# Kernel tuning notes

Hardware: AMD Instinct MI355X
Metric: run time of the kernel (lower is better)

## Reference

```python
import jax, jax.numpy as jnp
import numpy as np

N, C, EMB_ROWS = 524288, 128, 32
SLOPE = 0.2  # leaky_relu negative slope


def setup_inputs() -> dict:
    key = jax.random.key(0)
    k1, k2, k3, k4, k5 = jax.random.split(key, 5)
    x = jax.random.normal(k1, (N, C), jnp.float32)
    perm = jax.random.permutation(k2, N)  # fixed stand-in for torch.randperm
    depth = jax.random.normal(k3, (EMB_ROWS, 128), jnp.float32)  # Embedding(32,128), N(0,1) init
    fan_in = 2 * C * 2
    bound = 1.0 / np.sqrt(fan_in)
    W = jax.random.uniform(k4, (C, 2 * C, 2), jnp.float32, -bound, bound)  # Conv1d weight (O,I,K)
    b = jax.random.uniform(k5, (C,), jnp.float32, -bound, bound)
    return {"x": x, "depth": depth, "W": W, "b": b, "perm": perm}


def reference(x, depth, W, b, perm):
    c = W.shape[0]
    x = x[perm]                      # random shuffle of rows
    x = x.T.reshape(1, c, -1)        # [1, C, N]
    i = 0
    # Python while over STATIC shapes -> unrolled at trace time (~log2(N) steps)
    while x.shape[-1] > 1:
        L = x.shape[-1]
        e = jnp.broadcast_to(depth[i].reshape(1, 128, 1), (1, 128, L))
        x = jnp.concatenate([x, e], axis=1)   # [1, 2C, L]
        x = jax.lax.conv_general_dilated(
            x, W, window_strides=(1,), padding="VALID",
            dimension_numbers=("NCH", "OIH", "NCH"))  # [1, C, L-1]
        x = x + b.reshape(1, -1, 1)
        x = jnp.where(x >= 0, x, SLOPE * x)   # leaky_relu(0.2)
        if x.shape[-1] == 1:
            break
        # MaxPool1d(2,2): floor(L/2), drops trailing element for odd L
        x = jax.lax.reduce_window(
            x, -jnp.inf, jax.lax.max,
            window_dimensions=(1, 1, 2), window_strides=(1, 1, 2),
            padding="VALID")
        i += 1
    return x.reshape(c, 1).T  # [1, C]
```

## Files before the change

kernel.cpp:

```cpp
#include <hip/hip_runtime.h>
#include <hip/hip_bf16.h>


typedef __bf16 v8bf __attribute__((ext_vector_type(8)));
typedef float v16f __attribute__((ext_vector_type(16)));

__device__ __forceinline__ ushort f2bf(float f) {
    __hip_bfloat16 h = __float2bfloat16(f);
    return *reinterpret_cast<ushort*>(&h);
}
__device__ __forceinline__ unsigned pack2(float lo, float hi) {
    return (unsigned)f2bf(lo) | ((unsigned)f2bf(hi) << 16);
}
__device__ __forceinline__ float leaky(float y) { return (y >= 0.f) ? y : 0.2f * y; }

#define ZACC {0.f,0.f,0.f,0.f,0.f,0.f,0.f,0.f,0.f,0.f,0.f,0.f,0.f,0.f,0.f,0.f}

__global__ void bias_kernel(const float* __restrict__ W, const float* __restrict__ b,
                            const float* __restrict__ depth, float* __restrict__ Bst) {
    int i = blockIdx.x, o = threadIdx.x;
    const float* Wo = W + (size_t)o * 512 + 256;
    const float* di = depth + (size_t)i * 128;
    float s = b[o];
#pragma unroll 8
    for (int c = 0; c < 128; ++c) s += di[c] * (Wo[2 * c] + Wo[2 * c + 1]);
    Bst[i * 128 + o] = s;
}

__global__ void repack_kernel(const float* __restrict__ W, ushort* __restrict__ A) {
    int o = blockIdx.x, c = threadIdx.x;
    float v = (c < 128) ? W[(size_t)o * 512 + 2 * c] : W[(size_t)o * 512 + 2 * (c - 128) + 1];
    A[o * 256 + c] = f2bf(v);
}

#define WAVE_SETUP()                                                          \
    const int tid = threadIdx.x;                                              \
    const int lane = tid & 63;                                                \
    const int w = tid >> 6;                                                   \
    const int n31 = lane & 31;                                                \
    const int h = lane >> 5;                                                  \
    v8bf af[16];                                                              \
    {                                                                         \
        const ushort* Arow = A + (size_t)(w * 32 + n31) * 256 + h * 8;        \
        _Pragma("unroll")                                                     \
        for (int s = 0; s < 16; ++s) af[s] = *(const v8bf*)&Arow[s * 16];     \
    }

#define LOAD_BIAS(dst_, Bs)                                                   \
    float dst_[16];                                                           \
    _Pragma("unroll")                                                         \
    for (int r = 0; r < 16; ++r)                                              \
        dst_[r] = (Bs)[w * 32 + (r & 3) + 8 * (r >> 2) + 4 * h];

#define MFMA_TILE_LDS(buf, r0_, r1_, acc)                                     \
    {                                                                         \
        const ushort* sp0 = (buf) + (r0_) * 128;                              \
        const ushort* sp1 = (buf) + (r1_) * 128;                              \
        const int mm0 = (r0_) & 15, mm1 = (r1_) & 15;                         \
        v16f accB_ = ZACC;                                                    \
        __builtin_amdgcn_s_setprio(1);                                        \
        _Pragma("unroll")                                                     \
        for (int s = 0; s < 8; ++s) {                                         \
            acc = __builtin_amdgcn_mfma_f32_32x32x16_bf16(                    \
                af[s], *(const v8bf*)&sp0[((2 * s + h) ^ mm0) * 8], acc, 0, 0, 0); \
            accB_ = __builtin_amdgcn_mfma_f32_32x32x16_bf16(                  \
                af[8 + s], *(const v8bf*)&sp1[((2 * s + h) ^ mm1) * 8], accB_, 0, 0, 0); \
        }                                                                     \
        __builtin_amdgcn_s_setprio(0);                                        \
        acc += accB_;                                                         \
    }

__global__ __launch_bounds__(256)
void pair_fused(const ushort* __restrict__ Xin,
                const float* __restrict__ x0,
                const int* __restrict__ perm,
                const ushort* __restrict__ A,
                const float* __restrict__ Bst2,
                ushort* __restrict__ Y,
                int Lin, int Lp2, int stage0) {
    __shared__ __align__(16) ushort xin[132 * 128];
    __shared__ __align__(16) ushort mid[65 * 128];

    const int U = blockIdx.x * 32;
    const int t0 = U * 4;

    if (stage0) {
        int pr[9];
        float4 aa[9], bb[9];
#pragma unroll
        for (int k = 0; k < 9; ++k) {
            int idx = threadIdx.x + 256 * k;
            if (idx < 132 * 16) {
                int row = idx >> 4;
                pr[k] = perm[min(t0 + row, Lin - 1)];
            }
        }
#pragma unroll
        for (int k = 0; k < 9; ++k) {
            int idx = threadIdx.x + 256 * k;
            if (idx < 132 * 16) {
                int ck = idx & 15;
                const float* s = x0 + (size_t)pr[k] * 128 + ck * 8;
                aa[k] = *(const float4*)s;
                bb[k] = *(const float4*)(s + 4);
            }
        }
#pragma unroll
        for (int k = 0; k < 9; ++k) {
            int idx = threadIdx.x + 256 * k;
            if (idx < 132 * 16) {
                int row = idx >> 4, ck = idx & 15;
                uint4 v;
                v.x = pack2(aa[k].x, aa[k].y);  v.y = pack2(aa[k].z, aa[k].w);
                v.z = pack2(bb[k].x, bb[k].y);  v.w = pack2(bb[k].z, bb[k].w);
                *(uint4*)&xin[row * 128 + ((ck ^ (row & 15)) * 8)] = v;
            }
        }
    } else {
        uint4 vv[9];
#pragma unroll
        for (int k = 0; k < 9; ++k) {
            int idx = threadIdx.x + 256 * k;
            if (idx < 132 * 16) {
                int row = idx >> 4, ck = idx & 15;
                int t = min(t0 + row, Lin - 1);
                vv[k] = *(const uint4*)&Xin[(size_t)t * 128 + ck * 8];
            }
        }
#pragma unroll
        for (int k = 0; k < 9; ++k) {
            int idx = threadIdx.x + 256 * k;
            if (idx < 132 * 16) {
                int row = idx >> 4, ck = idx & 15;
                *(uint4*)&xin[row * 128 + ((ck ^ (row & 15)) * 8)] = vv[k];
            }
        }
    }
    __syncthreads();

    WAVE_SETUP();

    {
        LOAD_BIAS(bias_r, Bst2);
#pragma unroll
        for (int ti = 0; ti < 5; ++ti) {
            const int p = 32 * ti + n31;
            const int r0 = min(p, 131), r1 = min(p + 1, 131);
            v16f acc = ZACC;
            MFMA_TILE_LDS(xin, r0, r1, acc);
            const int u1 = 16 * ti + (n31 >> 1);
            const bool act = !(lane & 1) && (u1 < 65);
#pragma unroll
            for (int q = 0; q < 4; ++q) {
                float pv[4];
#pragma unroll
                for (int j = 0; j < 4; ++j) {
                    float y = leaky(acc[4 * q + j] + bias_r[4 * q + j]);
                    float y2 = __shfl_xor(y, 1, 64);
                    pv[j] = fmaxf(y, y2);
                }
                if (act) {
                    uint2 v;
                    v.x = pack2(pv[0], pv[1]);
                    v.y = pack2(pv[2], pv[3]);
                    *(uint2*)&mid[u1 * 128 + (((4 * w + q) ^ (u1 & 15)) * 8) + 4 * h] = v;
                }
            }
        }
    }
    __syncthreads();

    {
        LOAD_BIAS(bias_r, Bst2 + 128);
#pragma unroll
        for (int ti = 0; ti < 2; ++ti) {
            const int p = 32 * ti + n31;
            v16f acc = ZACC;
            MFMA_TILE_LDS(mid, p, p + 1, acc);
            const int u2 = U + 16 * ti + (n31 >> 1);
            const bool act = !(lane & 1) && (u2 < Lp2);
#pragma unroll
            for (int q = 0; q < 4; ++q) {
                float pv[4];
#pragma unroll
                for (int j = 0; j < 4; ++j) {
                    float y = leaky(acc[4 * q + j] + bias_r[4 * q + j]);
                    float y2 = __shfl_xor(y, 1, 64);
                    pv[j] = fmaxf(y, y2);
                }
                if (act) {
                    uint2 v;
                    v.x = pack2(pv[0], pv[1]);
                    v.y = pack2(pv[2], pv[3]);
                    *(uint2*)&Y[(size_t)u2 * 128 + w * 32 + 8 * q + 4 * h] = v;
                }
            }
        }
    }
}

__global__ __launch_bounds__(256)
void tail_fused(const ushort* __restrict__ Xg, const ushort* __restrict__ A,
                const float* __restrict__ BstAll, float* __restrict__ out) {
    extern __shared__ __align__(16) ushort tbuf[];
    ushort* buf0 = tbuf;
    ushort* buf1 = tbuf + 255 * 128;

    WAVE_SETUP();

    int Lin = 511;
    for (int st = 0; st < 8; ++st) {
        const int Lp = (Lin - 1) >> 1;
        LOAD_BIAS(bias_r, BstAll + (size_t)(10 + st) * 128);
        ushort* dst = (st & 1) ? buf1 : buf0;
        const ushort* src = (st & 1) ? buf0 : buf1;
        const int ntiles = (Lin - 1 + 31) >> 5;
        for (int ti = 0; ti < ntiles; ++ti) {
            const int t = ti * 32 + n31;
            const int r0 = min(t, Lin - 1), r1 = min(t + 1, Lin - 1);
            v16f acc = ZACC;
            if (st == 0) {
                const ushort* p0 = Xg + (size_t)r0 * 128 + h * 8;
                const ushort* p1 = Xg + (size_t)r1 * 128 + h * 8;
                v16f accB = ZACC;
                __builtin_amdgcn_s_setprio(1);
#pragma unroll
                for (int s = 0; s < 8; ++s) {
                    acc = __builtin_amdgcn_mfma_f32_32x32x16_bf16(
                        af[s], *(const v8bf*)&p0[s * 16], acc, 0, 0, 0);
                    accB = __builtin_amdgcn_mfma_f32_32x32x16_bf16(
                        af[8 + s], *(const v8bf*)&p1[s * 16], accB, 0, 0, 0);
                }
                __builtin_amdgcn_s_setprio(0);
                acc += accB;
            } else {
                MFMA_TILE_LDS(src, r0, r1, acc);
            }
            const int u = t >> 1;
            const bool act = !(lane & 1) && (u < Lp);
#pragma unroll
            for (int q = 0; q < 4; ++q) {
                float pv[4];
#pragma unroll
                for (int j = 0; j < 4; ++j) {
                    float y = leaky(acc[4 * q + j] + bias_r[4 * q + j]);
                    float y2 = __shfl_xor(y, 1, 64);
                    pv[j] = fmaxf(y, y2);
                }
                if (act) {
                    if (st < 7) {
                        uint2 v;
                        v.x = pack2(pv[0], pv[1]);
                        v.y = pack2(pv[2], pv[3]);
                        *(uint2*)&dst[u * 128 + (((4 * w + q) ^ (u & 15)) * 8) + 4 * h] = v;
                    } else {
                        float4 o = {pv[0], pv[1], pv[2], pv[3]};
                        *(float4*)&out[w * 32 + 8 * q + 4 * h] = o;
                    }
                }
            }
        }
        __syncthreads();
        Lin = Lp;
    }
}

extern "C" void kernel_launch(void* const* d_in, const int* in_sizes, int n_in,
                              void* d_out, int out_size, void* d_ws, size_t ws_size,
                              hipStream_t stream) {
    const float* x     = (const float*)d_in[0];
    const float* depth = (const float*)d_in[1];
    const float* W     = (const float*)d_in[2];
    const float* b     = (const float*)d_in[3];
    const int*   perm  = (const int*)d_in[4];
    float* out = (float*)d_out;

    char* ws = (char*)d_ws;
    float*  Bst = (float*)ws;
    ushort* A   = (ushort*)(ws + 16384);
    ushort* R0  = (ushort*)(ws + 16384 + 65536);
    ushort* R1  = (ushort*)(ws + 16384 + 65536 + (size_t)131071 * 256);

    bias_kernel<<<18, 128, 0, stream>>>(W, b, depth, Bst);
    repack_kernel<<<128, 256, 0, stream>>>(W, A);

    pair_fused<<<4096, 256, 0, stream>>>(nullptr, x, perm, A, Bst, R0,
                                         524288, 131071, 1);
    pair_fused<<<1024, 256, 0, stream>>>(R0, nullptr, nullptr, A, Bst + 2 * 128, R1,
                                         131071, 32767, 0);
    pair_fused<<<256, 256, 0, stream>>>(R1, nullptr, nullptr, A, Bst + 4 * 128, R0,
                                        32767, 8191, 0);
    pair_fused<<<64, 256, 0, stream>>>(R0, nullptr, nullptr, A, Bst + 6 * 128, R1,
                                       8191, 2047, 0);
    pair_fused<<<16, 256, 0, stream>>>(R1, nullptr, nullptr, A, Bst + 8 * 128, R0,
                                       2047, 511, 0);
    tail_fused<<<1, 256, (255 + 127) * 128 * 2, stream>>>(R0, A, Bst, out);
}
```

Before: 572.5 us.

## Pre-convert input to bf16, merge prep kernels, widen tail kernel

Adds a streaming pass that converts the whole fp32 input to bf16 before the first fused stage, so the permuted gather reads half as many bytes per row. It also stages perm indices in shared memory, merges the bias and weight repack kernels into one launch, drops s_setprio hints, and doubles the tail kernel's waves so tiles are split between two wave groups. The trade-off is an extra full read of x plus a 128MB write and re-read of the bf16 copy, which may cost more than it saves in the gather.

```diff
diff --git a/kernel.cpp b/kernel.cpp
--- a/kernel.cpp
+++ b/kernel.cpp
@@ -4,6 +4,7 @@
 
 typedef __bf16 v8bf __attribute__((ext_vector_type(8)));
 typedef float v16f __attribute__((ext_vector_type(16)));
+typedef float v4f __attribute__((ext_vector_type(4)));
 
 __device__ __forceinline__ ushort f2bf(float f) {
     __hip_bfloat16 h = __float2bfloat16(f);
@@ -16,41 +17,58 @@
 
 #define ZACC {0.f,0.f,0.f,0.f,0.f,0.f,0.f,0.f,0.f,0.f,0.f,0.f,0.f,0.f,0.f,0.f}
 
-__global__ void bias_kernel(const float* __restrict__ W, const float* __restrict__ b,
-                            const float* __restrict__ depth, float* __restrict__ Bst) {
-    int i = blockIdx.x, o = threadIdx.x;
-    const float* Wo = W + (size_t)o * 512 + 256;
-    const float* di = depth + (size_t)i * 128;
-    float s = b[o];
+__global__ __launch_bounds__(256)
+void prep_kernel(const float* __restrict__ W, const float* __restrict__ b,
+                 const float* __restrict__ depth, float* __restrict__ Bst,
+                 ushort* __restrict__ A) {
+    if (blockIdx.x < 18) {
+        if (threadIdx.x < 128) {
+            int i = blockIdx.x, o = threadIdx.x;
+            const float* Wo = W + (size_t)o * 512 + 256;
+            const float* di = depth + (size_t)i * 128;
+            float s = b[o];
 #pragma unroll 8
-    for (int c = 0; c < 128; ++c) s += di[c] * (Wo[2 * c] + Wo[2 * c + 1]);
-    Bst[i * 128 + o] = s;
-}
-
-__global__ void repack_kernel(const float* __restrict__ W, ushort* __restrict__ A) {
-    int o = blockIdx.x, c = threadIdx.x;
-    float v = (c < 128) ? W[(size_t)o * 512 + 2 * c] : W[(size_t)o * 512 + 2 * (c - 128) + 1];
-    A[o * 256 + c] = f2bf(v);
-}
-
-#define WAVE_SETUP()                                                          \
-    const int tid = threadIdx.x;                                              \
-    const int lane = tid & 63;                                                \
-    const int w = tid >> 6;                                                   \
-    const int n31 = lane & 31;                                                \
-    const int h = lane >> 5;                                                  \
+            for (int c = 0; c < 128; ++c) s += di[c] * (Wo[2 * c] + Wo[2 * c + 1]);
+            Bst[i * 128 + o] = s;
+        }
+    } else {
+        int o = blockIdx.x - 18, c = threadIdx.x;
+        float v = (c < 128) ? W[(size_t)o * 512 + 2 * c]
+                            : W[(size_t)o * 512 + 2 * (c - 128) + 1];
+        A[o * 256 + c] = f2bf(v);
+    }
+}
+
+__global__ __launch_bounds__(256)
+void convert_kernel(const float* __restrict__ x, ushort* __restrict__ Gx) {
+    const size_t nchunk = (size_t)524288 * 16;
+    const size_t stride = (size_t)gridDim.x * 256;
+    size_t i = (size_t)blockIdx.x * 256 + threadIdx.x;
+#pragma unroll 4
+    for (; i < nchunk; i += stride) {
+        const v4f* src = (const v4f*)(x + i * 8);
+        v4f a = __builtin_nontemporal_load(src);
+        v4f c = __builtin_nontemporal_load(src + 1);
+        uint4 v;
+        v.x = pack2(a.x, a.y);  v.y = pack2(a.z, a.w);
+        v.z = pack2(c.x, c.y);  v.w = pack2(c.z, c.w);
+        *(uint4*)(Gx + i * 8) = v;
+    }
+}
+
+#define WAVE_FRAG(WCH)                                                        \
     v8bf af[16];                                                              \
     {                                                                         \
-        const ushort* Arow = A + (size_t)(w * 32 + n31) * 256 + h * 8;        \
+        const ushort* Arow = A + (size_t)((WCH) * 32 + n31) * 256 + h * 8;    \
         _Pragma("unroll")                                                     \
         for (int s = 0; s < 16; ++s) af[s] = *(const v8bf*)&Arow[s * 16];     \
     }
 
-#define LOAD_BIAS(dst_, Bs)                                                   \
+#define LOAD_BIAS(dst_, Bs, WCH)                                              \
     float dst_[16];                                                           \
     _Pragma("unroll")                                                         \
     for (int r = 0; r < 16; ++r)                                              \
-        dst_[r] = (Bs)[w * 32 + (r & 3) + 8 * (r >> 2) + 4 * h];
+        dst_[r] = (Bs)[(WCH) * 32 + (r & 3) + 8 * (r >> 2) + 4 * h];
 
 #define MFMA_TILE_LDS(buf, r0_, r1_, acc)                                     \
     {                                                                         \
@@ -58,7 +76,6 @@
         const ushort* sp1 = (buf) + (r1_) * 128;                              \
         const int mm0 = (r0_) & 15, mm1 = (r1_) & 15;                         \
         v16f accB_ = ZACC;                                                    \
-        __builtin_amdgcn_s_setprio(1);                                        \
         _Pragma("unroll")                                                     \
         for (int s = 0; s < 8; ++s) {                                         \
             acc = __builtin_amdgcn_mfma_f32_32x32x16_bf16(                    \
@@ -66,82 +83,56 @@
             accB_ = __builtin_amdgcn_mfma_f32_32x32x16_bf16(                  \
                 af[8 + s], *(const v8bf*)&sp1[((2 * s + h) ^ mm1) * 8], accB_, 0, 0, 0); \
         }                                                                     \
-        __builtin_amdgcn_s_setprio(0);                                        \
         acc += accB_;                                                         \
     }
 
 __global__ __launch_bounds__(256)
 void pair_fused(const ushort* __restrict__ Xin,
-                const float* __restrict__ x0,
                 const int* __restrict__ perm,
                 const ushort* __restrict__ A,
                 const float* __restrict__ Bst2,
                 ushort* __restrict__ Y,
-                int Lin, int Lp2, int stage0) {
+                int Lin, int Lp2) {
     __shared__ __align__(16) ushort xin[132 * 128];
     __shared__ __align__(16) ushort mid[65 * 128];
+    __shared__ int prow[132];
 
     const int U = blockIdx.x * 32;
     const int t0 = U * 4;
 
-    if (stage0) {
-        int pr[9];
-        float4 aa[9], bb[9];
-#pragma unroll
-        for (int k = 0; k < 9; ++k) {
-            int idx = threadIdx.x + 256 * k;
-            if (idx < 132 * 16) {
-                int row = idx >> 4;
-                pr[k] = perm[min(t0 + row, Lin - 1)];
-            }
-        }
-#pragma unroll
-        for (int k = 0; k < 9; ++k) {
-            int idx = threadIdx.x + 256 * k;
-            if (idx < 132 * 16) {
-                int ck = idx & 15;
-                const float* s = x0 + (size_t)pr[k] * 128 + ck * 8;
-                aa[k] = *(const float4*)s;
-                bb[k] = *(const float4*)(s + 4);
-            }
-        }
-#pragma unroll
-        for (int k = 0; k < 9; ++k) {
-            int idx = threadIdx.x + 256 * k;
-            if (idx < 132 * 16) {
-                int row = idx >> 4, ck = idx & 15;
-                uint4 v;
-                v.x = pack2(aa[k].x, aa[k].y);  v.y = pack2(aa[k].z, aa[k].w);
-                v.z = pack2(bb[k].x, bb[k].y);  v.w = pack2(bb[k].z, bb[k].w);
-                *(uint4*)&xin[row * 128 + ((ck ^ (row & 15)) * 8)] = v;
-            }
-        }
-    } else {
-        uint4 vv[9];
-#pragma unroll
-        for (int k = 0; k < 9; ++k) {
-            int idx = threadIdx.x + 256 * k;
-            if (idx < 132 * 16) {
-                int row = idx >> 4, ck = idx & 15;
-                int t = min(t0 + row, Lin - 1);
-                vv[k] = *(const uint4*)&Xin[(size_t)t * 128 + ck * 8];
-            }
-        }
-#pragma unroll
-        for (int k = 0; k < 9; ++k) {
-            int idx = threadIdx.x + 256 * k;
-            if (idx < 132 * 16) {
-                int row = idx >> 4, ck = idx & 15;
-                *(uint4*)&xin[row * 128 + ((ck ^ (row & 15)) * 8)] = vv[k];
-            }
+    if (perm) {
+        int tix = threadIdx.x;
+        if (tix < 132) prow[tix] = perm[min(t0 + tix, Lin - 1)];
+        __syncthreads();
+    }
+    uint4 vv[9];
+#pragma unroll
+    for (int k = 0; k < 9; ++k) {
+        int idx = (int)threadIdx.x + 256 * k;
+        if (idx < 132 * 16) {
+            int row = idx >> 4;
+            int rs = perm ? prow[row] : min(t0 + row, Lin - 1);
+            vv[k] = *(const uint4*)&Xin[(size_t)rs * 128 + (idx & 15) * 8];
+        }
+    }
+#pragma unroll
+    for (int k = 0; k < 9; ++k) {
+        int idx = (int)threadIdx.x + 256 * k;
+        if (idx < 132 * 16) {
+            int row = idx >> 4, ck = idx & 15;
+            *(uint4*)&xin[row * 128 + ((ck ^ (row & 15)) * 8)] = vv[k];
         }
     }
     __syncthreads();
 
-    WAVE_SETUP();
+    const int lane = threadIdx.x & 63;
+    const int w = threadIdx.x >> 6;
+    const int n31 = lane & 31;
+    const int h = lane >> 5;
+    WAVE_FRAG(w);
 
     {
-        LOAD_BIAS(bias_r, Bst2);
+        LOAD_BIAS(bias_r, Bst2, w);
 #pragma unroll
         for (int ti = 0; ti < 5; ++ti) {
             const int p = 32 * ti + n31;
@@ -171,7 +162,7 @@
     __syncthreads();
 
     {
-        LOAD_BIAS(bias_r, Bst2 + 128);
+        LOAD_BIAS(bias_r, Bst2 + 128, w);
 #pragma unroll
         for (int ti = 0; ti < 2; ++ti) {
             const int p = 32 * ti + n31;
@@ -199,23 +190,29 @@
     }
 }
 
-__global__ __launch_bounds__(256)
+__global__ __launch_bounds__(512)
 void tail_fused(const ushort* __restrict__ Xg, const ushort* __restrict__ A,
                 const float* __restrict__ BstAll, float* __restrict__ out) {
     extern __shared__ __align__(16) ushort tbuf[];
     ushort* buf0 = tbuf;
     ushort* buf1 = tbuf + 255 * 128;
 
-    WAVE_SETUP();
+    const int lane = threadIdx.x & 63;
+    const int w = threadIdx.x >> 6;
+    const int wq = w & 3;
+    const int wp = w >> 2;
+    const int n31 = lane & 31;
+    const int h = lane >> 5;
+    WAVE_FRAG(wq);
 
     int Lin = 511;
     for (int st = 0; st < 8; ++st) {
         const int Lp = (Lin - 1) >> 1;
-        LOAD_BIAS(bias_r, BstAll + (size_t)(10 + st) * 128);
+        LOAD_BIAS(bias_r, BstAll + (size_t)(10 + st) * 128, wq);
         ushort* dst = (st & 1) ? buf1 : buf0;
         const ushort* src = (st & 1) ? buf0 : buf1;
         const int ntiles = (Lin - 1 + 31) >> 5;
-        for (int ti = 0; ti < ntiles; ++ti) {
+        for (int ti = wp; ti < ntiles; ti += 2) {
             const int t = ti * 32 + n31;
             const int r0 = min(t, Lin - 1), r1 = min(t + 1, Lin - 1);
             v16f acc = ZACC;
@@ -223,7 +220,6 @@
                 const ushort* p0 = Xg + (size_t)r0 * 128 + h * 8;
                 const ushort* p1 = Xg + (size_t)r1 * 128 + h * 8;
                 v16f accB = ZACC;
-                __builtin_amdgcn_s_setprio(1);
 #pragma unroll
                 for (int s = 0; s < 8; ++s) {
                     acc = __builtin_amdgcn_mfma_f32_32x32x16_bf16(
@@ -231,7 +227,6 @@
                     accB = __builtin_amdgcn_mfma_f32_32x32x16_bf16(
                         af[8 + s], *(const v8bf*)&p1[s * 16], accB, 0, 0, 0);
                 }
-                __builtin_amdgcn_s_setprio(0);
                 acc += accB;
             } else {
                 MFMA_TILE_LDS(src, r0, r1, acc);
@@ -252,10 +247,10 @@
                         uint2 v;
                         v.x = pack2(pv[0], pv[1]);
                         v.y = pack2(pv[2], pv[3]);
-                        *(uint2*)&dst[u * 128 + (((4 * w + q) ^ (u & 15)) * 8) + 4 * h] = v;
+                        *(uint2*)&dst[u * 128 + (((4 * wq + q) ^ (u & 15)) * 8) + 4 * h] = v;
                     } else {
                         float4 o = {pv[0], pv[1], pv[2], pv[3]};
-                        *(float4*)&out[w * 32 + 8 * q + 4 * h] = o;
+                        *(float4*)&out[wq * 32 + 8 * q + 4 * h] = o;
                     }
                 }
             }
@@ -278,21 +273,17 @@
     char* ws = (char*)d_ws;
     float*  Bst = (float*)ws;
     ushort* A   = (ushort*)(ws + 16384);
-    ushort* R0  = (ushort*)(ws + 16384 + 65536);
-    ushort* R1  = (ushort*)(ws + 16384 + 65536 + (size_t)131071 * 256);
-
-    bias_kernel<<<18, 128, 0, stream>>>(W, b, depth, Bst);
-    repack_kernel<<<128, 256, 0, stream>>>(W, A);
-
-    pair_fused<<<4096, 256, 0, stream>>>(nullptr, x, perm, A, Bst, R0,
-                                         524288, 131071, 1);
-    pair_fused<<<1024, 256, 0, stream>>>(R0, nullptr, nullptr, A, Bst + 2 * 128, R1,
-                                         131071, 32767, 0);
-    pair_fused<<<256, 256, 0, stream>>>(R1, nullptr, nullptr, A, Bst + 4 * 128, R0,
-                                        32767, 8191, 0);
-    pair_fused<<<64, 256, 0, stream>>>(R0, nullptr, nullptr, A, Bst + 6 * 128, R1,
-                                       8191, 2047, 0);
-    pair_fused<<<16, 256, 0, stream>>>(R1, nullptr, nullptr, A, Bst + 8 * 128, R0,
-                                       2047, 511, 0);
-    tail_fused<<<1, 256, (255 + 127) * 128 * 2, stream>>>(R0, A, Bst, out);
-}
+    ushort* Gx  = (ushort*)(ws + 16384 + 65536);
+    ushort* R0  = (ushort*)(ws + 16384 + 65536 + (size_t)134217728);
+    ushort* R1  = (ushort*)(ws + 16384 + 65536 + (size_t)134217728 + (size_t)131071 * 256);
+
+    prep_kernel<<<146, 256, 0, stream>>>(W, b, depth, Bst, A);
+    convert_kernel<<<8192, 256, 0, stream>>>(x, Gx);
+
+    pair_fused<<<4096, 256, 0, stream>>>(Gx, perm, A, Bst, R0, 524288, 131071);
+    pair_fused<<<1024, 256, 0, stream>>>(R0, nullptr, A, Bst + 2 * 128, R1, 131071, 32767);
+    pair_fused<<<256, 256, 0, stream>>>(R1, nullptr, A, Bst + 4 * 128, R0, 32767, 8191);
+    pair_fused<<<64, 256, 0, stream>>>(R0, nullptr, A, Bst + 6 * 128, R1, 8191, 2047);
+    pair_fused<<<16, 256, 0, stream>>>(R1, nullptr, A, Bst + 8 * 128, R0, 2047, 511);
+    tail_fused<<<1, 512, (255 + 127) * 128 * 2, stream>>>(R0, A, Bst, out);
+}
```

New measurement: 638.9 us. +11.6%, slower.
